# Kernel tuning notes

Hardware: AMD Instinct MI355X
Metric: run time of the kernel (lower is better)

Reference implementation:

```python
import jax, jax.numpy as jnp
import numpy as np

DIM = 256
N_EMBED = 8192
DECAY = 0.99
EPS = 1e-05


def setup_inputs() -> dict:
    key = jax.random.key(0)
    k1, k2, k3, k4 = jax.random.split(key, 4)
    z = jax.random.normal(k1, (16, 32, 32, DIM), dtype=jnp.float32)
    embedding = jax.random.normal(k2, (DIM, N_EMBED), dtype=jnp.float32)
    cluster_size = jax.random.uniform(k3, (N_EMBED,), dtype=jnp.float32)
    embedding_avg = jax.random.normal(k4, (DIM, N_EMBED), dtype=jnp.float32)
    return {"z": z, "embedding": embedding, "cluster_size": cluster_size,
            "embedding_avg": embedding_avg}


def reference(z, embedding, cluster_size, embedding_avg):
    flatten = z.reshape(-1, DIM)  # [N, dim]
    dist = ((flatten ** 2).sum(1, keepdims=True)
            - 2.0 * flatten @ embedding
            + (embedding ** 2).sum(0, keepdims=True))
    embed_ind_flat = jnp.argmin(dist, axis=1)  # [N] int
    embed_ind = embed_ind_flat.reshape(z.shape[:-1])
    # Gather codes: embedding is [dim, n_embed]; quantize [..., dim]
    quantize = jnp.take(embedding.T, embed_ind_flat, axis=0).reshape(z.shape)

    # EMA codebook update (training path), via segment sums (no dense one-hot)
    onehot_sum = jax.ops.segment_sum(
        jnp.ones_like(embed_ind_flat, dtype=flatten.dtype),
        embed_ind_flat, num_segments=N_EMBED)  # [n_embed]
    embed_sum = jax.ops.segment_sum(flatten, embed_ind_flat,
                                    num_segments=N_EMBED).T  # [dim, n_embed]
    new_cluster_size = cluster_size * DECAY + (1.0 - DECAY) * onehot_sum
    new_embedding_avg = embedding_avg * DECAY + (1.0 - DECAY) * embed_sum
    n = new_cluster_size.sum()
    smoothed = (new_cluster_size + EPS) / (n + N_EMBED * EPS) * n
    new_embedding = new_embedding_avg / smoothed[None, :]

    diff = jnp.mean((jax.lax.stop_gradient(quantize) - z) ** 2)
    quantize_st = z + jax.lax.stop_gradient(quantize - z)
    return (quantize_st, diff, embed_ind, new_embedding,
            new_cluster_size, new_embedding_avg)
```

## Files before the change

kernel.cpp:

```cpp
#include <hip/hip_runtime.h>


#define DIMC  256
#define NEMB  8192
#define NROWS 16384

#define OUT_Q      0u
#define OUT_DIFF   4194304u
#define OUT_IDX    4194305u
#define OUT_NEWEMB 4210689u
#define OUT_NEWCS  6307841u
#define OUT_NEWAVG 6316033u

#define WS_EHI    0u
#define WS_ELO    1048576u
#define WS_COUNT  2097152u
#define WS_DIFF   2105344u
#define WS_N      2105345u
#define WS_ENORM  2105346u
#define WS_IDX    2113538u
#define WS_PACK_F 2129922u

typedef __attribute__((ext_vector_type(8))) short short8;
typedef __attribute__((ext_vector_type(4))) float f32x4;

__device__ inline void split_bf16(float x, unsigned short& h, unsigned short& l) {
  unsigned u = __float_as_uint(x);
  unsigned r = u + 0x7FFFu + ((u >> 16) & 1u);
  h = (unsigned short)(r >> 16);
  float hf = __uint_as_float((unsigned)h << 16);
  float lo = x - hf;
  unsigned u2 = __float_as_uint(lo);
  unsigned r2 = u2 + 0x7FFFu + ((u2 >> 16) & 1u);
  l = (unsigned short)(r2 >> 16);
}

__global__ __launch_bounds__(256) void prep_z_kernel(
    const float* __restrict__ z, unsigned short* __restrict__ z_hi,
    unsigned short* __restrict__ z_lo) {
  const int idx = blockIdx.x * 256 + threadIdx.x;
  const float4 v = reinterpret_cast<const float4*>(z)[idx];
  ushort4 h, l;
  split_bf16(v.x, h.x, l.x);
  split_bf16(v.y, h.y, l.y);
  split_bf16(v.z, h.z, l.z);
  split_bf16(v.w, h.w, l.w);
  reinterpret_cast<ushort4*>(z_hi)[idx] = h;
  reinterpret_cast<ushort4*>(z_lo)[idx] = l;
}

__global__ __launch_bounds__(256) void prep_emb_kernel(
    const float* __restrict__ emb, unsigned short* __restrict__ e_hi,
    unsigned short* __restrict__ e_lo, float* __restrict__ embt) {
  __shared__ float tile[64][68];
  const int t = threadIdx.x;
  const int n0 = blockIdx.x * 64;
  const int k0 = blockIdx.y * 64;
  const int c4 = (t & 15) * 4;
  const int rr = t >> 4;
#pragma unroll
  for (int i = 0; i < 4; ++i) {
    const int kl = rr + i * 16;
    const float4 v = *reinterpret_cast<const float4*>(
        &emb[(size_t)(k0 + kl) * NEMB + n0 + c4]);
    *reinterpret_cast<float4*>(&tile[kl][c4]) = v;
  }
  __syncthreads();
#pragma unroll
  for (int i = 0; i < 4; ++i) {
    const int nr = rr + i * 16;
    float4 v;
    v.x = tile[c4 + 0][nr];
    v.y = tile[c4 + 1][nr];
    v.z = tile[c4 + 2][nr];
    v.w = tile[c4 + 3][nr];
    const size_t off = (size_t)(n0 + nr) * DIMC + k0 + c4;
    *reinterpret_cast<float4*>(&embt[off]) = v;
    ushort4 h, l;
    split_bf16(v.x, h.x, l.x);
    split_bf16(v.y, h.y, l.y);
    split_bf16(v.z, h.z, l.z);
    split_bf16(v.w, h.w, l.w);
    *reinterpret_cast<ushort4*>(&e_hi[off]) = h;
    *reinterpret_cast<ushort4*>(&e_lo[off]) = l;
  }
}

__global__ __launch_bounds__(256) void enorm_kernel(
    const float* __restrict__ emb, float* __restrict__ enorm) {
  __shared__ float red[4][64];
  const int l = threadIdx.x & 63;
  const int dg = threadIdx.x >> 6;
  const int e = blockIdx.x * 64 + l;
  float s = 0.f;
#pragma unroll 8
  for (int d = dg * 64; d < dg * 64 + 64; ++d) {
    const float v = emb[(size_t)d * NEMB + e];
    s = fmaf(v, v, s);
  }
  red[dg][l] = s;
  __syncthreads();
  if (dg == 0) enorm[e] = red[0][l] + red[1][l] + red[2][l] + red[3][l];
}

__global__ __launch_bounds__(256, 2) void argmin_mfma_kernel(
    const unsigned short* __restrict__ z_hi, const unsigned short* __restrict__ z_lo,
    const unsigned short* __restrict__ e_hi, const unsigned short* __restrict__ e_lo,
    const float* __restrict__ enorm, unsigned long long* __restrict__ pack) {
  __shared__ short za[16384];
  __shared__ short eb[16384];
  const int tid = threadIdx.x;
  const int bid = blockIdx.x;
  const int r0 = (bid >> 2) * 128;
  const int ebase = (bid & 3) * 2048;
  const int tx = tid & 15;
  const int q = (tid >> 4) & 3;
  const int wave = tid >> 6;
  const int wm = wave & 1;
  const int wn = wave >> 1;

  float rmin[4][4];
  int ridx[4][4];
#pragma unroll
  for (int i = 0; i < 4; ++i)
#pragma unroll
    for (int r = 0; r < 4; ++r) { rmin[i][r] = 3.4028235e38f; ridx[i][r] = 0; }

  for (int nt = 0; nt < 16; ++nt) {
    const int n0 = ebase + nt * 128;
    f32x4 acc[4][4];
#pragma unroll
    for (int i = 0; i < 4; ++i)
#pragma unroll
      for (int j = 0; j < 4; ++j) acc[i][j] = (f32x4)0.0f;

    for (int kt = 0; kt < 4; ++kt) {
      const int k0 = kt * 64;
      __syncthreads();
#pragma unroll
      for (int it = 0; it < 8; ++it) {
        const int P = tid + it * 256;
        const int row = P >> 4;
        const int p = P & 15;
        const int o = (p & 7) ^ (row & 7);
        const unsigned short* zsrc =
            ((p & 8) ? z_lo : z_hi) + (size_t)(r0 + row) * DIMC + k0 + o * 8;
        __builtin_amdgcn_global_load_lds(
            (const __attribute__((address_space(1))) unsigned int*)zsrc,
            (__attribute__((address_space(3))) unsigned int*)&za[P * 8], 16, 0, 0);
        const unsigned short* esrc =
            ((p & 8) ? e_lo : e_hi) + (size_t)(n0 + row) * DIMC + k0 + o * 8;
        __builtin_amdgcn_global_load_lds(
            (const __attribute__((address_space(1))) unsigned int*)esrc,
            (__attribute__((address_space(3))) unsigned int*)&eb[P * 8], 16, 0, 0);
      }
      __syncthreads();
#pragma unroll
      for (int ks = 0; ks < 2; ++ks) {
        short8 ah[4], al[4], bh[4], bl[4];
#pragma unroll
        for (int i = 0; i < 4; ++i) {
          const int rl = wm * 64 + i * 16 + tx;
          const int oa = (ks * 4 + q) ^ (rl & 7);
          ah[i] = *reinterpret_cast<const short8*>(&za[rl * 128 + oa * 8]);
          al[i] = *reinterpret_cast<const short8*>(&za[rl * 128 + (oa + 8) * 8]);
          const int cl = wn * 64 + i * 16 + tx;
          const int ob = (ks * 4 + q) ^ (cl & 7);
          bh[i] = *reinterpret_cast<const short8*>(&eb[cl * 128 + ob * 8]);
          bl[i] = *reinterpret_cast<const short8*>(&eb[cl * 128 + (ob + 8) * 8]);
        }
#pragma unroll
        for (int i = 0; i < 4; ++i)
#pragma unroll
          for (int j = 0; j < 4; ++j) {
            acc[i][j] = __builtin_amdgcn_mfma_f32_16x16x32_bf16(ah[i], bh[j],
                                                               acc[i][j], 0, 0, 0);
            acc[i][j] = __builtin_amdgcn_mfma_f32_16x16x32_bf16(ah[i], bl[j],
                                                               acc[i][j], 0, 0, 0);
            acc[i][j] = __builtin_amdgcn_mfma_f32_16x16x32_bf16(al[i], bh[j],
                                                               acc[i][j], 0, 0, 0);
          }
      }
    }
#pragma unroll
    for (int j = 0; j < 4; ++j) {
      const int col = n0 + wn * 64 + j * 16 + tx;
      const float en = enorm[col];
#pragma unroll
      for (int i = 0; i < 4; ++i)
#pragma unroll
        for (int r = 0; r < 4; ++r) {
          const float s = en - 2.0f * acc[i][j][r];
          if (s < rmin[i][r]) { rmin[i][r] = s; ridx[i][r] = col; }
        }
    }
  }
#pragma unroll
  for (int i = 0; i < 4; ++i)
#pragma unroll
    for (int r = 0; r < 4; ++r) {
      float v = rmin[i][r];
      int ix = ridx[i][r];
#pragma unroll
      for (int off = 1; off < 16; off <<= 1) {
        const float ov = __shfl_xor(v, off, 64);
        const int oi = __shfl_xor(ix, off, 64);
        if (ov < v || (ov == v && oi < ix)) { v = ov; ix = oi; }
      }
      if (tx == 0) {
        const unsigned int fb = __float_as_uint(v);
        const unsigned int sb = (fb & 0x80000000u) ? ~fb : (fb | 0x80000000u);
        const unsigned long long key =
            ((unsigned long long)sb << 13) | (unsigned long long)(unsigned)ix;
        atomicMin(&pack[r0 + wm * 64 + i * 16 + q * 4 + r], key);
      }
    }
}

__global__ __launch_bounds__(256) void extract_idx_kernel(
    const unsigned long long* __restrict__ pack, float* __restrict__ out_idx,
    int* __restrict__ ws_idx) {
  const int r = blockIdx.x * 256 + threadIdx.x;
  const int e = (int)(pack[r] & 8191ULL);
  out_idx[r] = (float)e;
  ws_idx[r] = e;
}

__global__ __launch_bounds__(256) void gather_update_kernel(
    const float* __restrict__ z, const float* __restrict__ embt,
    const int* __restrict__ ws_idx, float* __restrict__ out_q,
    float* __restrict__ embsum, float* __restrict__ count,
    float* __restrict__ diff_acc) {
  const int row = blockIdx.x * 4 + (threadIdx.x >> 6);
  const int lane = threadIdx.x & 63;
  const int e = ws_idx[row];
  const float4 zv =
      *reinterpret_cast<const float4*>(&z[(size_t)row * DIMC + lane * 4]);
  const float4 qv =
      *reinterpret_cast<const float4*>(&embt[(size_t)e * DIMC + lane * 4]);
  const float d0 = qv.x - zv.x, d1 = qv.y - zv.y, d2 = qv.z - zv.z,
              d3 = qv.w - zv.w;
  float4 st;
  st.x = zv.x + d0; st.y = zv.y + d1; st.z = zv.z + d2; st.w = zv.w + d3;
  *reinterpret_cast<float4*>(&out_q[(size_t)row * DIMC + lane * 4]) = st;

  atomicAdd(&embsum[(size_t)e * DIMC + lane * 4 + 0], zv.x);
  atomicAdd(&embsum[(size_t)e * DIMC + lane * 4 + 1], zv.y);
  atomicAdd(&embsum[(size_t)e * DIMC + lane * 4 + 2], zv.z);
  atomicAdd(&embsum[(size_t)e * DIMC + lane * 4 + 3], zv.w);

  float local = d0 * d0 + d1 * d1 + d2 * d2 + d3 * d3;
#pragma unroll
  for (int off = 32; off > 0; off >>= 1) local += __shfl_down(local, off, 64);

  __shared__ float dred[4];
  if (lane == 0) {
    dred[threadIdx.x >> 6] = local;
    atomicAdd(&count[e], 1.0f);
  }
  __syncthreads();
  if (threadIdx.x == 0)
    atomicAdd(diff_acc, dred[0] + dred[1] + dred[2] + dred[3]);
}

__global__ __launch_bounds__(256) void finalize_cluster_kernel(
    const float* __restrict__ cs, const float* __restrict__ count,
    float* __restrict__ out_ncs, float* __restrict__ out_diff,
    const float* __restrict__ diff_acc, float* __restrict__ n_acc) {
  const int g = blockIdx.x * 256 + threadIdx.x;
  const float ncs = cs[g] * 0.99f + 0.01f * count[g];
  out_ncs[g] = ncs;
  float s = ncs;
#pragma unroll
  for (int off = 32; off > 0; off >>= 1) s += __shfl_down(s, off, 64);
  __shared__ float red[4];
  const int w = threadIdx.x >> 6;
  if ((threadIdx.x & 63) == 0) red[w] = s;
  __syncthreads();
  if (threadIdx.x == 0) atomicAdd(n_acc, red[0] + red[1] + red[2] + red[3]);
  if (g == 0) out_diff[0] = diff_acc[0] * (1.0f / 4194304.0f);
}

__global__ __launch_bounds__(256) void finalize1_kernel(
    const float* __restrict__ eavg, const float* __restrict__ embsum,
    float* __restrict__ avgtmp) {
  __shared__ float tile[64][68];
  const int t = threadIdx.x;
  const int e0 = blockIdx.x * 64;
  const int d0 = blockIdx.y * 64;
  const int c4 = (t & 15) * 4;
  const int rr = t >> 4;
#pragma unroll
  for (int i = 0; i < 4; ++i) {
    const int er = rr + i * 16;
    const float4 v = *reinterpret_cast<const float4*>(
        &embsum[(size_t)(e0 + er) * DIMC + d0 + c4]);
    *reinterpret_cast<float4*>(&tile[er][c4]) = v;
  }
  __syncthreads();
#pragma unroll
  for (int i = 0; i < 4; ++i) {
    const int dr = rr + i * 16;
    const size_t g = (size_t)(d0 + dr) * NEMB + e0 + c4;
    const float4 av = *reinterpret_cast<const float4*>(&eavg[g]);
    float4 o;
    o.x = av.x * 0.99f + 0.01f * tile[c4 + 0][dr];
    o.y = av.y * 0.99f + 0.01f * tile[c4 + 1][dr];
    o.z = av.z * 0.99f + 0.01f * tile[c4 + 2][dr];
    o.w = av.w * 0.99f + 0.01f * tile[c4 + 3][dr];
    *reinterpret_cast<float4*>(&avgtmp[g]) = o;
  }
}

__global__ __launch_bounds__(256) void finalize2_kernel(
    const float* __restrict__ ncs_out, const float* __restrict__ n_acc,
    float* __restrict__ out_avg, float* __restrict__ out_emb_and_avgtmp) {
  const int g = blockIdx.x * 256 + threadIdx.x;
  const int e = g & 8191;
  const float avg = out_emb_and_avgtmp[g];
  const float n = n_acc[0];
  const float ncs = ncs_out[e];
  const float smoothed = (ncs + 1e-5f) / (n + (float)NEMB * 1e-5f) * n;
  out_avg[g] = avg;
  out_emb_and_avgtmp[g] = avg / smoothed;
}

extern "C" void kernel_launch(void* const* d_in, const int* in_sizes, int n_in,
                              void* d_out, int out_size, void* d_ws,
                              size_t ws_size, hipStream_t stream) {
  const float* z = (const float*)d_in[0];
  const float* emb = (const float*)d_in[1];
  const float* cs = (const float*)d_in[2];
  const float* eavg = (const float*)d_in[3];
  float* out = (float*)d_out;
  float* ws = (float*)d_ws;

  unsigned short* e_hi = (unsigned short*)(ws + WS_EHI);
  unsigned short* e_lo = (unsigned short*)(ws + WS_ELO);
  float* ws_count = ws + WS_COUNT;
  float* ws_diff = ws + WS_DIFF;
  float* ws_n = ws + WS_N;
  float* ws_enorm = ws + WS_ENORM;
  int* ws_idx = (int*)(ws + WS_IDX);
  unsigned long long* ws_pack = (unsigned long long*)(ws + WS_PACK_F);

  unsigned short* z_hi = (unsigned short*)(out + OUT_Q);
  unsigned short* z_lo = (unsigned short*)(out + OUT_Q + 2097152);
  float* embt = out + OUT_NEWEMB;
  float* embsum = out + OUT_NEWAVG;

  hipMemsetAsync(ws_count, 0, (size_t)(NEMB + 2) * sizeof(float), stream);
  hipMemsetAsync(ws_pack, 0xFF, (size_t)NROWS * sizeof(unsigned long long),
                 stream);
  hipMemsetAsync(embsum, 0, (size_t)NEMB * DIMC * sizeof(float), stream);

  prep_z_kernel<<<4096, 256, 0, stream>>>(z, z_hi, z_lo);
  prep_emb_kernel<<<dim3(NEMB / 64, DIMC / 64), 256, 0, stream>>>(emb, e_hi,
                                                                  e_lo, embt);
  enorm_kernel<<<NEMB / 64, 256, 0, stream>>>(emb, ws_enorm);
  argmin_mfma_kernel<<<512, 256, 0, stream>>>(z_hi, z_lo, e_hi, e_lo, ws_enorm,
                                              ws_pack);
  extract_idx_kernel<<<NROWS / 256, 256, 0, stream>>>(ws_pack, out + OUT_IDX,
                                                      ws_idx);
  gather_update_kernel<<<NROWS / 4, 256, 0, stream>>>(
      z, embt, ws_idx, out + OUT_Q, embsum, ws_count, ws_diff);
  finalize_cluster_kernel<<<NEMB / 256, 256, 0, stream>>>(
      cs, ws_count, out + OUT_NEWCS, out + OUT_DIFF, ws_diff, ws_n);
  finalize1_kernel<<<dim3(NEMB / 64, DIMC / 64), 256, 0, stream>>>(
      eavg, embsum, embt );
  finalize2_kernel<<<(DIMC * NEMB) / 256, 256, 0, stream>>>(
      out + OUT_NEWCS, ws_n, out + OUT_NEWAVG ,
      embt );
}
```

Baseline: 414.8 us.

## Merge prep kernels, drop transposed fp32 codebook, fuse index extraction into gather

Combines the z split, codebook split, embedding-norm and embsum zeroing into one launch, replacing a large memset, and merges the cluster finalize into the avg finalize launch. The gather now rebuilds quantized vectors from the bf16 hi/lo pair instead of writing and reading a transposed fp32 codebook copy. It also reads the argmin index straight from the packed key, removing the extract kernel. The shuffle width in the argmin reduction is narrowed to 16. The hi+lo reconstruction may differ slightly from the exact fp32 codebook values, which could affect quantize_st and diff precision.

Result: faster. 396.0 us (-4.6%).

```diff
diff --git a/kernel.cpp b/kernel.cpp
--- a/kernel.cpp
+++ b/kernel.cpp
@@ -18,8 +18,7 @@
 #define WS_DIFF   2105344u
 #define WS_N      2105345u
 #define WS_ENORM  2105346u
-#define WS_IDX    2113538u
-#define WS_PACK_F 2129922u
+#define WS_PACK   2113540u
 
 typedef __attribute__((ext_vector_type(8))) short short8;
 typedef __attribute__((ext_vector_type(4))) float f32x4;
@@ -35,72 +34,84 @@
   l = (unsigned short)(r2 >> 16);
 }
 
-__global__ __launch_bounds__(256) void prep_z_kernel(
-    const float* __restrict__ z, unsigned short* __restrict__ z_hi,
-    unsigned short* __restrict__ z_lo) {
-  const int idx = blockIdx.x * 256 + threadIdx.x;
-  const float4 v = reinterpret_cast<const float4*>(z)[idx];
-  ushort4 h, l;
-  split_bf16(v.x, h.x, l.x);
-  split_bf16(v.y, h.y, l.y);
-  split_bf16(v.z, h.z, l.z);
-  split_bf16(v.w, h.w, l.w);
-  reinterpret_cast<ushort4*>(z_hi)[idx] = h;
-  reinterpret_cast<ushort4*>(z_lo)[idx] = l;
-}
-
-__global__ __launch_bounds__(256) void prep_emb_kernel(
-    const float* __restrict__ emb, unsigned short* __restrict__ e_hi,
-    unsigned short* __restrict__ e_lo, float* __restrict__ embt) {
+__device__ inline float bf16_f(unsigned short u) {
+  return __uint_as_float((unsigned)u << 16);
+}
+
+__global__ __launch_bounds__(256) void prep_kernel(
+    const float* __restrict__ z, const float* __restrict__ emb,
+    unsigned short* __restrict__ z_hi, unsigned short* __restrict__ z_lo,
+    unsigned short* __restrict__ e_hi, unsigned short* __restrict__ e_lo,
+    float* __restrict__ enorm, float* __restrict__ embsum) {
+  const int b = blockIdx.x;
+  const int t = threadIdx.x;
   __shared__ float tile[64][68];
-  const int t = threadIdx.x;
-  const int n0 = blockIdx.x * 64;
-  const int k0 = blockIdx.y * 64;
-  const int c4 = (t & 15) * 4;
-  const int rr = t >> 4;
-#pragma unroll
-  for (int i = 0; i < 4; ++i) {
-    const int kl = rr + i * 16;
-    const float4 v = *reinterpret_cast<const float4*>(
-        &emb[(size_t)(k0 + kl) * NEMB + n0 + c4]);
-    *reinterpret_cast<float4*>(&tile[kl][c4]) = v;
+  __shared__ float red[4][64];
+
+  if (b < 1024) {
+#pragma unroll
+    for (int it = 0; it < 4; ++it) {
+      const int idx = (b * 256 + t) + it * 262144;
+      const float4 v = reinterpret_cast<const float4*>(z)[idx];
+      ushort4 h, l;
+      split_bf16(v.x, h.x, l.x);
+      split_bf16(v.y, h.y, l.y);
+      split_bf16(v.z, h.z, l.z);
+      split_bf16(v.w, h.w, l.w);
+      reinterpret_cast<ushort4*>(z_hi)[idx] = h;
+      reinterpret_cast<ushort4*>(z_lo)[idx] = l;
+    }
+  } else if (b < 1536) {
+    const int bb = b - 1024;
+    const int n0 = (bb & 127) * 64;
+    const int k0 = (bb >> 7) * 64;
+    const int c4 = (t & 15) * 4;
+    const int rr = t >> 4;
+#pragma unroll
+    for (int i = 0; i < 4; ++i) {
+      const int kl = rr + i * 16;
+      const float4 v = *reinterpret_cast<const float4*>(
+          &emb[(size_t)(k0 + kl) * NEMB + n0 + c4]);
+      *reinterpret_cast<float4*>(&tile[kl][c4]) = v;
+    }
+    __syncthreads();
+#pragma unroll
+    for (int i = 0; i < 4; ++i) {
+      const int nr = rr + i * 16;
+      float4 v;
+      v.x = tile[c4 + 0][nr];
+      v.y = tile[c4 + 1][nr];
+      v.z = tile[c4 + 2][nr];
+      v.w = tile[c4 + 3][nr];
+      const size_t off = (size_t)(n0 + nr) * DIMC + k0 + c4;
+      ushort4 h, l;
+      split_bf16(v.x, h.x, l.x);
+      split_bf16(v.y, h.y, l.y);
+      split_bf16(v.z, h.z, l.z);
+      split_bf16(v.w, h.w, l.w);
+      *reinterpret_cast<ushort4*>(&e_hi[off]) = h;
+      *reinterpret_cast<ushort4*>(&e_lo[off]) = l;
+    }
+  } else if (b < 2048) {
+    const int bb = b - 1536;
+    const float4 zero = {0.f, 0.f, 0.f, 0.f};
+#pragma unroll
+    for (int it = 0; it < 4; ++it)
+      reinterpret_cast<float4*>(embsum)[bb * 1024 + t + it * 256] = zero;
+  } else {
+    const int l = t & 63;
+    const int dg = t >> 6;
+    const int e = (b - 2048) * 64 + l;
+    float s = 0.f;
+#pragma unroll 8
+    for (int d = dg * 64; d < dg * 64 + 64; ++d) {
+      const float v = emb[(size_t)d * NEMB + e];
+      s = fmaf(v, v, s);
+    }
+    red[dg][l] = s;
+    __syncthreads();
+    if (dg == 0) enorm[e] = red[0][l] + red[1][l] + red[2][l] + red[3][l];
   }
-  __syncthreads();
-#pragma unroll
-  for (int i = 0; i < 4; ++i) {
-    const int nr = rr + i * 16;
-    float4 v;
-    v.x = tile[c4 + 0][nr];
-    v.y = tile[c4 + 1][nr];
-    v.z = tile[c4 + 2][nr];
-    v.w = tile[c4 + 3][nr];
-    const size_t off = (size_t)(n0 + nr) * DIMC + k0 + c4;
-    *reinterpret_cast<float4*>(&embt[off]) = v;
-    ushort4 h, l;
-    split_bf16(v.x, h.x, l.x);
-    split_bf16(v.y, h.y, l.y);
-    split_bf16(v.z, h.z, l.z);
-    split_bf16(v.w, h.w, l.w);
-    *reinterpret_cast<ushort4*>(&e_hi[off]) = h;
-    *reinterpret_cast<ushort4*>(&e_lo[off]) = l;
-  }
-}
-
-__global__ __launch_bounds__(256) void enorm_kernel(
-    const float* __restrict__ emb, float* __restrict__ enorm) {
-  __shared__ float red[4][64];
-  const int l = threadIdx.x & 63;
-  const int dg = threadIdx.x >> 6;
-  const int e = blockIdx.x * 64 + l;
-  float s = 0.f;
-#pragma unroll 8
-  for (int d = dg * 64; d < dg * 64 + 64; ++d) {
-    const float v = emb[(size_t)d * NEMB + e];
-    s = fmaf(v, v, s);
-  }
-  red[dg][l] = s;
-  __syncthreads();
-  if (dg == 0) enorm[e] = red[0][l] + red[1][l] + red[2][l] + red[3][l];
 }
 
 __global__ __launch_bounds__(256, 2) void argmin_mfma_kernel(
@@ -203,8 +214,8 @@
       int ix = ridx[i][r];
 #pragma unroll
       for (int off = 1; off < 16; off <<= 1) {
-        const float ov = __shfl_xor(v, off, 64);
-        const int oi = __shfl_xor(ix, off, 64);
+        const float ov = __shfl_xor(v, off, 16);
+        const int oi = __shfl_xor(ix, off, 16);
         if (ov < v || (ov == v && oi < ix)) { v = ov; ix = oi; }
       }
       if (tx == 0) {
@@ -217,29 +228,27 @@
     }
 }
 
-__global__ __launch_bounds__(256) void extract_idx_kernel(
-    const unsigned long long* __restrict__ pack, float* __restrict__ out_idx,
-    int* __restrict__ ws_idx) {
-  const int r = blockIdx.x * 256 + threadIdx.x;
-  const int e = (int)(pack[r] & 8191ULL);
-  out_idx[r] = (float)e;
-  ws_idx[r] = e;
-}
-
 __global__ __launch_bounds__(256) void gather_update_kernel(
-    const float* __restrict__ z, const float* __restrict__ embt,
-    const int* __restrict__ ws_idx, float* __restrict__ out_q,
-    float* __restrict__ embsum, float* __restrict__ count,
-    float* __restrict__ diff_acc) {
+    const float* __restrict__ z, const unsigned short* __restrict__ e_hi,
+    const unsigned short* __restrict__ e_lo,
+    const unsigned long long* __restrict__ pack, float* __restrict__ out_q,
+    float* __restrict__ out_idx, float* __restrict__ embsum,
+    float* __restrict__ count, float* __restrict__ diff_acc) {
   const int row = blockIdx.x * 4 + (threadIdx.x >> 6);
   const int lane = threadIdx.x & 63;
-  const int e = ws_idx[row];
+  const int e = (int)(pack[row] & 8191ULL);
+  if (lane == 0) out_idx[row] = (float)e;
   const float4 zv =
       *reinterpret_cast<const float4*>(&z[(size_t)row * DIMC + lane * 4]);
-  const float4 qv =
-      *reinterpret_cast<const float4*>(&embt[(size_t)e * DIMC + lane * 4]);
-  const float d0 = qv.x - zv.x, d1 = qv.y - zv.y, d2 = qv.z - zv.z,
-              d3 = qv.w - zv.w;
+  const ushort4 h =
+      *reinterpret_cast<const ushort4*>(&e_hi[(size_t)e * DIMC + lane * 4]);
+  const ushort4 l =
+      *reinterpret_cast<const ushort4*>(&e_lo[(size_t)e * DIMC + lane * 4]);
+  const float q0 = bf16_f(h.x) + bf16_f(l.x);
+  const float q1 = bf16_f(h.y) + bf16_f(l.y);
+  const float q2 = bf16_f(h.z) + bf16_f(l.z);
+  const float q3 = bf16_f(h.w) + bf16_f(l.w);
+  const float d0 = q0 - zv.x, d1 = q1 - zv.y, d2 = q2 - zv.z, d3 = q3 - zv.w;
   float4 st;
   st.x = zv.x + d0; st.y = zv.y + d1; st.z = zv.z + d2; st.w = zv.w + d3;
   *reinterpret_cast<float4*>(&out_q[(size_t)row * DIMC + lane * 4]) = st;
@@ -263,56 +272,56 @@
     atomicAdd(diff_acc, dred[0] + dred[1] + dred[2] + dred[3]);
 }
 
-__global__ __launch_bounds__(256) void finalize_cluster_kernel(
-    const float* __restrict__ cs, const float* __restrict__ count,
-    float* __restrict__ out_ncs, float* __restrict__ out_diff,
-    const float* __restrict__ diff_acc, float* __restrict__ n_acc) {
-  const int g = blockIdx.x * 256 + threadIdx.x;
-  const float ncs = cs[g] * 0.99f + 0.01f * count[g];
-  out_ncs[g] = ncs;
-  float s = ncs;
-#pragma unroll
-  for (int off = 32; off > 0; off >>= 1) s += __shfl_down(s, off, 64);
-  __shared__ float red[4];
-  const int w = threadIdx.x >> 6;
-  if ((threadIdx.x & 63) == 0) red[w] = s;
-  __syncthreads();
-  if (threadIdx.x == 0) atomicAdd(n_acc, red[0] + red[1] + red[2] + red[3]);
-  if (g == 0) out_diff[0] = diff_acc[0] * (1.0f / 4194304.0f);
-}
-
-__global__ __launch_bounds__(256) void finalize1_kernel(
+__global__ __launch_bounds__(256) void fin_a_kernel(
     const float* __restrict__ eavg, const float* __restrict__ embsum,
-    float* __restrict__ avgtmp) {
+    float* __restrict__ avgtmp, const float* __restrict__ cs,
+    const float* __restrict__ count, float* __restrict__ out_ncs,
+    float* __restrict__ out_diff, const float* __restrict__ diff_acc,
+    float* __restrict__ n_acc) {
+  const int b = blockIdx.x;
+  const int t = threadIdx.x;
   __shared__ float tile[64][68];
-  const int t = threadIdx.x;
-  const int e0 = blockIdx.x * 64;
-  const int d0 = blockIdx.y * 64;
-  const int c4 = (t & 15) * 4;
-  const int rr = t >> 4;
-#pragma unroll
-  for (int i = 0; i < 4; ++i) {
-    const int er = rr + i * 16;
-    const float4 v = *reinterpret_cast<const float4*>(
-        &embsum[(size_t)(e0 + er) * DIMC + d0 + c4]);
-    *reinterpret_cast<float4*>(&tile[er][c4]) = v;
+  if (b < 512) {
+    const int e0 = (b & 127) * 64;
+    const int d0 = (b >> 7) * 64;
+    const int c4 = (t & 15) * 4;
+    const int rr = t >> 4;
+#pragma unroll
+    for (int i = 0; i < 4; ++i) {
+      const int er = rr + i * 16;
+      const float4 v = *reinterpret_cast<const float4*>(
+          &embsum[(size_t)(e0 + er) * DIMC + d0 + c4]);
+      *reinterpret_cast<float4*>(&tile[er][c4]) = v;
+    }
+    __syncthreads();
+#pragma unroll
+    for (int i = 0; i < 4; ++i) {
+      const int dr = rr + i * 16;
+      const size_t g = (size_t)(d0 + dr) * NEMB + e0 + c4;
+      const float4 av = *reinterpret_cast<const float4*>(&eavg[g]);
+      float4 o;
+      o.x = av.x * 0.99f + 0.01f * tile[c4 + 0][dr];
+      o.y = av.y * 0.99f + 0.01f * tile[c4 + 1][dr];
+      o.z = av.z * 0.99f + 0.01f * tile[c4 + 2][dr];
+      o.w = av.w * 0.99f + 0.01f * tile[c4 + 3][dr];
+      *reinterpret_cast<float4*>(&avgtmp[g]) = o;
+    }
+  } else {
+    const int g = (b - 512) * 256 + t;
+    const float ncs = cs[g] * 0.99f + 0.01f * count[g];
+    out_ncs[g] = ncs;
+    float s = ncs;
+#pragma unroll
+    for (int off = 32; off > 0; off >>= 1) s += __shfl_down(s, off, 64);
+    __shared__ float red[4];
+    if ((t & 63) == 0) red[t >> 6] = s;
+    __syncthreads();
+    if (t == 0) atomicAdd(n_acc, red[0] + red[1] + red[2] + red[3]);
+    if (g == 0) out_diff[0] = diff_acc[0] * (1.0f / 4194304.0f);
   }
-  __syncthreads();
-#pragma unroll
-  for (int i = 0; i < 4; ++i) {
-    const int dr = rr + i * 16;
-    const size_t g = (size_t)(d0 + dr) * NEMB + e0 + c4;
-    const float4 av = *reinterpret_cast<const float4*>(&eavg[g]);
-    float4 o;
-    o.x = av.x * 0.99f + 0.01f * tile[c4 + 0][dr];
-    o.y = av.y * 0.99f + 0.01f * tile[c4 + 1][dr];
-    o.z = av.z * 0.99f + 0.01f * tile[c4 + 2][dr];
-    o.w = av.w * 0.99f + 0.01f * tile[c4 + 3][dr];
-    *reinterpret_cast<float4*>(&avgtmp[g]) = o;
-  }
-}
-
-__global__ __launch_bounds__(256) void finalize2_kernel(
+}
+
+__global__ __launch_bounds__(256) void fin2_kernel(
     const float* __restrict__ ncs_out, const float* __restrict__ n_acc,
     float* __restrict__ out_avg, float* __restrict__ out_emb_and_avgtmp) {
   const int g = blockIdx.x * 256 + threadIdx.x;
@@ -341,34 +350,27 @@
   float* ws_diff = ws + WS_DIFF;
   float* ws_n = ws + WS_N;
   float* ws_enorm = ws + WS_ENORM;
-  int* ws_idx = (int*)(ws + WS_IDX);
-  unsigned long long* ws_pack = (unsigned long long*)(ws + WS_PACK_F);
+  unsigned long long* ws_pack = (unsigned long long*)(ws + WS_PACK);
 
   unsigned short* z_hi = (unsigned short*)(out + OUT_Q);
   unsigned short* z_lo = (unsigned short*)(out + OUT_Q + 2097152);
-  float* embt = out + OUT_NEWEMB;
   float* embsum = out + OUT_NEWAVG;
-
-  hipMemsetAsync(ws_count, 0, (size_t)(NEMB + 2) * sizeof(float), stream);
+  float* avgtmp = out + OUT_NEWEMB;
+
+  hipMemsetAsync(ws_count, 0, (size_t)8194 * sizeof(float), stream);
   hipMemsetAsync(ws_pack, 0xFF, (size_t)NROWS * sizeof(unsigned long long),
                  stream);
-  hipMemsetAsync(embsum, 0, (size_t)NEMB * DIMC * sizeof(float), stream);
-
-  prep_z_kernel<<<4096, 256, 0, stream>>>(z, z_hi, z_lo);
-  prep_emb_kernel<<<dim3(NEMB / 64, DIMC / 64), 256, 0, stream>>>(emb, e_hi,
-                                                                  e_lo, embt);
-  enorm_kernel<<<NEMB / 64, 256, 0, stream>>>(emb, ws_enorm);
+
+  prep_kernel<<<2176, 256, 0, stream>>>(z, emb, z_hi, z_lo, e_hi, e_lo,
+                                        ws_enorm, embsum);
   argmin_mfma_kernel<<<512, 256, 0, stream>>>(z_hi, z_lo, e_hi, e_lo, ws_enorm,
                                               ws_pack);
-  extract_idx_kernel<<<NROWS / 256, 256, 0, stream>>>(ws_pack, out + OUT_IDX,
-                                                      ws_idx);
   gather_update_kernel<<<NROWS / 4, 256, 0, stream>>>(
-      z, embt, ws_idx, out + OUT_Q, embsum, ws_count, ws_diff);
-  finalize_cluster_kernel<<<NEMB / 256, 256, 0, stream>>>(
-      cs, ws_count, out + OUT_NEWCS, out + OUT_DIFF, ws_diff, ws_n);
-  finalize1_kernel<<<dim3(NEMB / 64, DIMC / 64), 256, 0, stream>>>(
-      eavg, embsum, embt );
-  finalize2_kernel<<<(DIMC * NEMB) / 256, 256, 0, stream>>>(
-      out + OUT_NEWCS, ws_n, out + OUT_NEWAVG ,
-      embt );
-}
+      z, e_hi, e_lo, ws_pack, out + OUT_Q, out + OUT_IDX, embsum, ws_count,
+      ws_diff);
+  fin_a_kernel<<<544, 256, 0, stream>>>(eavg, embsum, avgtmp, cs, ws_count,
+                                        out + OUT_NEWCS, out + OUT_DIFF,
+                                        ws_diff, ws_n);
+  fin2_kernel<<<(DIMC * NEMB) / 256, 256, 0, stream>>>(
+      out + OUT_NEWCS, ws_n, out + OUT_NEWAVG, avgtmp);
+}
```
